# Optimization experiments

Measured on AMD Instinct MI355X. Metric: run time of the kernel, lower is better.

## Reference

```python
import jax, jax.numpy as jnp
import numpy as np

B, D, F, T = 8192, 128, 128, 64


def setup_inputs() -> dict:
    key = jax.random.key(0)
    k1, k2, k3, k4 = jax.random.split(key, 4)
    inputs = jax.random.normal(k1, (B, D), dtype=jnp.float32)
    task_idx = jax.random.randint(k2, (B,), 0, T, dtype=jnp.int32)
    # default_kernel_init: normal * 1/sqrt(shape[1]) where shape=(T, D, F)
    kernels = jax.random.normal(k3, (T, D, F), dtype=jnp.float32) / jnp.sqrt(float(D))
    biases = jnp.zeros((T, F), dtype=jnp.float32)
    return {"inputs": inputs, "task_idx": task_idx, "kernels": kernels, "biases": biases}


def reference(inputs, task_idx, kernels, biases):
    # MoEDense forward (vector task_idx branch):
    #   y[b] = inputs[b] @ kernels[task_idx[b]] + biases[task_idx[b]]
    t = jnp.clip(task_idx, 0, kernels.shape[0] - 1)
    k_g = jnp.take(kernels, t, axis=0)          # [B, D, F] per-sample expert gather
    y = jnp.einsum('bd,bdf->bf', inputs, k_g)   # per-sample vec-mat
    y = y + jnp.take(biases, t, axis=0)
    return y
```

## Files before the change

### kernel.cpp

```cpp
#include <hip/hip_runtime.h>
#include <stdint.h>


#define D_ 128
#define F_ 128
#define T_ 64
#define TILE_M 32
#define TPE 16
#define LDA 136

typedef __attribute__((ext_vector_type(8))) short short8;
typedef __attribute__((ext_vector_type(8))) unsigned short ushort8;
typedef __attribute__((ext_vector_type(4))) float floatx4;

__device__ __forceinline__ int clamp_t(int t) {
    return t < 0 ? 0 : (t > T_ - 1 ? T_ - 1 : t);
}
__device__ __forceinline__ unsigned short f2bf(float f) {
    union { float f; unsigned u; } c; c.f = f;
    unsigned r = c.u + 0x7fffu + ((c.u >> 16) & 1u);
    return (unsigned short)(r >> 16);
}

__global__ __launch_bounds__(256) void moe_fused(
    const float* __restrict__ x,
    const int*   __restrict__ tidx,
    const float* __restrict__ kern,
    const float* __restrict__ bias,
    float*       __restrict__ out)
{
    const int e    = blockIdx.x >> 4;
    const int tb   = blockIdx.x & (TPE - 1);
    const int m0   = tb * TILE_M;
    const int tid  = threadIdx.x;
    const int wv   = tid >> 6;
    const int lane = tid & 63;

    __shared__ int wtot[4];
    __shared__ int slot[TILE_M];
    __shared__ __align__(16) unsigned short A[TILE_M * LDA];

    const int4* tp = reinterpret_cast<const int4*>(tidx) + tid * 8;
    int4 v[8];
    #pragma unroll
    for (int c = 0; c < 8; ++c) v[c] = tp[c];

    int my = 0;
    #pragma unroll
    for (int c = 0; c < 8; ++c) {
        my += (clamp_t(v[c].x) == e);
        my += (clamp_t(v[c].y) == e);
        my += (clamp_t(v[c].z) == e);
        my += (clamp_t(v[c].w) == e);
    }
    int pre = my;
    #pragma unroll
    for (int d = 1; d < 64; d <<= 1) {
        int u = __shfl_up(pre, d);
        if (lane >= d) pre += u;
    }
    if (lane == 63) wtot[wv] = pre;
    __syncthreads();
    int wbase = 0, cnt = 0;
    #pragma unroll
    for (int w = 0; w < 4; ++w) {
        const int t = wtot[w];
        if (w < wv) wbase += t;
        cnt += t;
    }
    if (m0 >= cnt) return;
    const int base = wbase + pre - my;

    if (base < m0 + TILE_M && base + my > m0) {
        int run = base;
        #pragma unroll
        for (int c = 0; c < 8; ++c) {
            const int row4 = tid * 32 + c * 4;
            const int tt[4] = { v[c].x, v[c].y, v[c].z, v[c].w };
            #pragma unroll
            for (int j = 0; j < 4; ++j) {
                if (clamp_t(tt[j]) == e) {
                    if (run >= m0 && run < m0 + TILE_M)
                        slot[run - m0] = row4 + j;
                    ++run;
                }
            }
        }
    }
    __syncthreads();

    {
        const int row = tid >> 3;
        const int c   = (tid & 7) * 16;
        const int r   = (m0 + row < cnt) ? slot[row] : -1;
        float4 v0 = {0.f,0.f,0.f,0.f}, v1 = v0, v2 = v0, v3 = v0;
        if (r >= 0) {
            const float4* xp = reinterpret_cast<const float4*>(x + r * D_ + c);
            v0 = xp[0]; v1 = xp[1]; v2 = xp[2]; v3 = xp[3];
        }
        ushort8 h0, h1;
        h0[0]=f2bf(v0.x); h0[1]=f2bf(v0.y); h0[2]=f2bf(v0.z); h0[3]=f2bf(v0.w);
        h0[4]=f2bf(v1.x); h0[5]=f2bf(v1.y); h0[6]=f2bf(v1.z); h0[7]=f2bf(v1.w);
        h1[0]=f2bf(v2.x); h1[1]=f2bf(v2.y); h1[2]=f2bf(v2.z); h1[3]=f2bf(v2.w);
        h1[4]=f2bf(v3.x); h1[5]=f2bf(v3.y); h1[6]=f2bf(v3.z); h1[7]=f2bf(v3.w);
        *reinterpret_cast<ushort8*>(&A[row * LDA + c])     = h0;
        *reinterpret_cast<ushort8*>(&A[row * LDA + c + 8]) = h1;
    }
    __syncthreads();

    const int quad = lane >> 4;
    const int l16  = lane & 15;
    const int n0   = wv * 32;

    floatx4 acc00 = {0.f,0.f,0.f,0.f}, acc01 = acc00, acc10 = acc00, acc11 = acc00;
    const float* Bp = kern + e * (D_ * F_);

    #pragma unroll
    for (int kc = 0; kc < 4; ++kc) {
        const int k0 = kc * 32;
        const short8 a0 = *reinterpret_cast<const short8*>(&A[l16 * LDA + k0 + quad * 8]);
        const short8 a1 = *reinterpret_cast<const short8*>(&A[(16 + l16) * LDA + k0 + quad * 8]);
        const float* bp = Bp + (k0 + quad * 8) * F_ + n0 + l16;
        short8 b0, b1;
        #pragma unroll
        for (int j = 0; j < 8; ++j) {
            b0[j] = (short)f2bf(bp[j * F_]);
            b1[j] = (short)f2bf(bp[j * F_ + 16]);
        }
        acc00 = __builtin_amdgcn_mfma_f32_16x16x32_bf16(a0, b0, acc00, 0, 0, 0);
        acc01 = __builtin_amdgcn_mfma_f32_16x16x32_bf16(a0, b1, acc01, 0, 0, 0);
        acc10 = __builtin_amdgcn_mfma_f32_16x16x32_bf16(a1, b0, acc10, 0, 0, 0);
        acc11 = __builtin_amdgcn_mfma_f32_16x16x32_bf16(a1, b1, acc11, 0, 0, 0);
    }

    const float bs0 = bias[e * F_ + n0 + l16];
    const float bs1 = bias[e * F_ + n0 + l16 + 16];
    #pragma unroll
    for (int reg = 0; reg < 4; ++reg) {
        const int mA = quad * 4 + reg;
        if (m0 + mA < cnt) {
            const int r = slot[mA];
            out[r * F_ + n0 + l16]      = acc00[reg] + bs0;
            out[r * F_ + n0 + l16 + 16] = acc01[reg] + bs1;
        }
        const int mB = 16 + mA;
        if (m0 + mB < cnt) {
            const int r = slot[mB];
            out[r * F_ + n0 + l16]      = acc10[reg] + bs0;
            out[r * F_ + n0 + l16 + 16] = acc11[reg] + bs1;
        }
    }
}

extern "C" void kernel_launch(void* const* d_in, const int* in_sizes, int n_in,
                              void* d_out, int out_size, void* d_ws, size_t ws_size,
                              hipStream_t stream) {
    const float* x    = (const float*)d_in[0];
    const int*   tidx = (const int*)d_in[1];
    const float* kern = (const float*)d_in[2];
    const float* bias = (const float*)d_in[3];
    float* out = (float*)d_out;
    (void)d_ws; (void)ws_size; (void)in_sizes; (void)n_in;

    moe_fused<<<T_ * TPE, 256, 0, stream>>>(x, tidx, kern, bias, out);
}
```

Measured before the change: 75.70 us.

## Pre-convert inputs to bf16 in a prep kernel and read A fragments from global

Adds a separate kernel that converts all inputs to bf16 in a workspace, so the main kernel drops the LDS staging of A, one barrier, and the per-tile fp32->bf16 conversion. It loads MFMA A fragments directly from the bf16 workspace using the gathered row indices. The task_idx loads are also changed to a coalesced strided pattern across threads. The cost is an extra kernel launch and a full write and re-read of a 2 MB bf16 copy of the inputs.

```diff
diff --git a/kernel.cpp b/kernel.cpp
--- a/kernel.cpp
+++ b/kernel.cpp
@@ -7,7 +7,6 @@
 #define T_ 64
 #define TILE_M 32
 #define TPE 16
-#define LDA 136
 
 typedef __attribute__((ext_vector_type(8))) short short8;
 typedef __attribute__((ext_vector_type(8))) unsigned short ushort8;
@@ -22,12 +21,24 @@
     return (unsigned short)(r >> 16);
 }
 
+__global__ __launch_bounds__(256) void moe_prep(
+    const float* __restrict__ x, unsigned short* __restrict__ ws)
+{
+    const int i0 = (blockIdx.x * 256 + threadIdx.x) * 8;
+    const float4* xp = reinterpret_cast<const float4*>(x + i0);
+    const float4 a = xp[0], b = xp[1];
+    ushort8 h;
+    h[0]=f2bf(a.x); h[1]=f2bf(a.y); h[2]=f2bf(a.z); h[3]=f2bf(a.w);
+    h[4]=f2bf(b.x); h[5]=f2bf(b.y); h[6]=f2bf(b.z); h[7]=f2bf(b.w);
+    *reinterpret_cast<ushort8*>(&ws[i0]) = h;
+}
+
 __global__ __launch_bounds__(256) void moe_fused(
-    const float* __restrict__ x,
-    const int*   __restrict__ tidx,
+    const int* __restrict__ tidx,
+    const unsigned short* __restrict__ ws,
     const float* __restrict__ kern,
     const float* __restrict__ bias,
-    float*       __restrict__ out)
+    float* __restrict__ out)
 {
     const int e    = blockIdx.x >> 4;
     const int tb   = blockIdx.x & (TPE - 1);
@@ -38,12 +49,11 @@
 
     __shared__ int wtot[4];
     __shared__ int slot[TILE_M];
-    __shared__ __align__(16) unsigned short A[TILE_M * LDA];
 
-    const int4* tp = reinterpret_cast<const int4*>(tidx) + tid * 8;
+    const int4* tp = reinterpret_cast<const int4*>(tidx);
     int4 v[8];
     #pragma unroll
-    for (int c = 0; c < 8; ++c) v[c] = tp[c];
+    for (int c = 0; c < 8; ++c) v[c] = tp[c * 256 + tid];
 
     int my = 0;
     #pragma unroll
@@ -75,7 +85,7 @@
         int run = base;
         #pragma unroll
         for (int c = 0; c < 8; ++c) {
-            const int row4 = tid * 32 + c * 4;
+            const int row4 = (c * 256 + tid) * 4;
             const int tt[4] = { v[c].x, v[c].y, v[c].z, v[c].w };
             #pragma unroll
             for (int j = 0; j < 4; ++j) {
@@ -89,28 +99,12 @@
     }
     __syncthreads();
 
-    {
-        const int row = tid >> 3;
-        const int c   = (tid & 7) * 16;
-        const int r   = (m0 + row < cnt) ? slot[row] : -1;
-        float4 v0 = {0.f,0.f,0.f,0.f}, v1 = v0, v2 = v0, v3 = v0;
-        if (r >= 0) {
-            const float4* xp = reinterpret_cast<const float4*>(x + r * D_ + c);
-            v0 = xp[0]; v1 = xp[1]; v2 = xp[2]; v3 = xp[3];
-        }
-        ushort8 h0, h1;
-        h0[0]=f2bf(v0.x); h0[1]=f2bf(v0.y); h0[2]=f2bf(v0.z); h0[3]=f2bf(v0.w);
-        h0[4]=f2bf(v1.x); h0[5]=f2bf(v1.y); h0[6]=f2bf(v1.z); h0[7]=f2bf(v1.w);
-        h1[0]=f2bf(v2.x); h1[1]=f2bf(v2.y); h1[2]=f2bf(v2.z); h1[3]=f2bf(v2.w);
-        h1[4]=f2bf(v3.x); h1[5]=f2bf(v3.y); h1[6]=f2bf(v3.z); h1[7]=f2bf(v3.w);
-        *reinterpret_cast<ushort8*>(&A[row * LDA + c])     = h0;
-        *reinterpret_cast<ushort8*>(&A[row * LDA + c + 8]) = h1;
-    }
-    __syncthreads();
-
     const int quad = lane >> 4;
     const int l16  = lane & 15;
-    const int n0   = wv * 32;
+    const int n0w  = wv * 32;
+
+    const int rA = (m0 + l16 < cnt)      ? slot[l16]      : 0;
+    const int rB = (m0 + 16 + l16 < cnt) ? slot[16 + l16] : 0;
 
     floatx4 acc00 = {0.f,0.f,0.f,0.f}, acc01 = acc00, acc10 = acc00, acc11 = acc00;
     const float* Bp = kern + e * (D_ * F_);
@@ -118,9 +112,9 @@
     #pragma unroll
     for (int kc = 0; kc < 4; ++kc) {
         const int k0 = kc * 32;
-        const short8 a0 = *reinterpret_cast<const short8*>(&A[l16 * LDA + k0 + quad * 8]);
-        const short8 a1 = *reinterpret_cast<const short8*>(&A[(16 + l16) * LDA + k0 + quad * 8]);
-        const float* bp = Bp + (k0 + quad * 8) * F_ + n0 + l16;
+        const short8 a0 = *reinterpret_cast<const short8*>(&ws[rA * D_ + k0 + quad * 8]);
+        const short8 a1 = *reinterpret_cast<const short8*>(&ws[rB * D_ + k0 + quad * 8]);
+        const float* bp = Bp + (k0 + quad * 8) * F_ + n0w + l16;
         short8 b0, b1;
         #pragma unroll
         for (int j = 0; j < 8; ++j) {
@@ -133,21 +127,21 @@
         acc11 = __builtin_amdgcn_mfma_f32_16x16x32_bf16(a1, b1, acc11, 0, 0, 0);
     }
 
-    const float bs0 = bias[e * F_ + n0 + l16];
-    const float bs1 = bias[e * F_ + n0 + l16 + 16];
+    const float bs0 = bias[e * F_ + n0w + l16];
+    const float bs1 = bias[e * F_ + n0w + l16 + 16];
     #pragma unroll
     for (int reg = 0; reg < 4; ++reg) {
         const int mA = quad * 4 + reg;
         if (m0 + mA < cnt) {
             const int r = slot[mA];
-            out[r * F_ + n0 + l16]      = acc00[reg] + bs0;
-            out[r * F_ + n0 + l16 + 16] = acc01[reg] + bs1;
+            out[r * F_ + n0w + l16]      = acc00[reg] + bs0;
+            out[r * F_ + n0w + l16 + 16] = acc01[reg] + bs1;
         }
         const int mB = 16 + mA;
         if (m0 + mB < cnt) {
             const int r = slot[mB];
-            out[r * F_ + n0 + l16]      = acc10[reg] + bs0;
-            out[r * F_ + n0 + l16 + 16] = acc11[reg] + bs1;
+            out[r * F_ + n0w + l16]      = acc10[reg] + bs0;
+            out[r * F_ + n0w + l16 + 16] = acc11[reg] + bs1;
         }
     }
 }
@@ -160,7 +154,9 @@
     const float* kern = (const float*)d_in[2];
     const float* bias = (const float*)d_in[3];
     float* out = (float*)d_out;
-    (void)d_ws; (void)ws_size; (void)in_sizes; (void)n_in;
+    unsigned short* wsu = (unsigned short*)d_ws;
+    (void)in_sizes; (void)n_in; (void)out_size; (void)ws_size;
 
-    moe_fused<<<T_ * TPE, 256, 0, stream>>>(x, tidx, kern, bias, out);
+    moe_prep <<<512,  256, 0, stream>>>(x, wsu);
+    moe_fused<<<T_ * TPE, 256, 0, stream>>>(tidx, wsu, kern, bias, out);
 }
```

Result: slower. 77.49 us (+2.4%).
